# Kernel tuning notes

Hardware: AMD Instinct MI355X
Metric: run time of the kernel (lower is better)

## Reference

```python
import jax, jax.numpy as jnp
import numpy as np

N = 100000
E = 1600000
D = 64
ED = 16
L = 3


def setup_inputs() -> dict:
    key = jax.random.key(0)
    ks = jax.random.split(key, 12)
    s = 1.0 / np.sqrt(D)
    se = 1.0 / np.sqrt(ED)
    return {
        "x": jax.random.normal(ks[0], (N, D), dtype=jnp.float32),
        "edge_index": jax.random.randint(ks[1], (2, E), 0, N, dtype=jnp.int64),
        "edge_attr": jax.random.normal(ks[2], (E, ED), dtype=jnp.float32),
        "Wk": jax.random.normal(ks[3], (L, D, D), dtype=jnp.float32) * s,
        "bk": jnp.zeros((L, D), dtype=jnp.float32),
        "Wq": jax.random.normal(ks[4], (L, D, D), dtype=jnp.float32) * s,
        "bq": jnp.zeros((L, D), dtype=jnp.float32),
        "Wv": jax.random.normal(ks[5], (L, D, D), dtype=jnp.float32) * s,
        "bv": jnp.zeros((L, D), dtype=jnp.float32),
        "We": jax.random.normal(ks[6], (L, ED, D), dtype=jnp.float32) * se,
        "be": jnp.zeros((L, D), dtype=jnp.float32),
        "Wskip": jax.random.normal(ks[7], (L, D, D), dtype=jnp.float32) * s,
        "bias": jnp.zeros((L, D), dtype=jnp.float32),
        "Wl": jax.random.normal(ks[8], (D, 1), dtype=jnp.float32) * s,
        "bl": jnp.zeros((1,), dtype=jnp.float32),
    }


def _res_gated_conv(h, src, dst, edge_attr, Wk, bk, Wq, bq, Wv, bv, We, be, Wskip, bias):
    # PyG ResGatedGraphConv: eta = sigmoid(k_i + q_j + lin_edge(e)); out_i = sum_j eta * v_j + lin_skip(x_i) + bias
    k = h @ Wk + bk            # [N, D]
    q = h @ Wq + bq            # [N, D]
    v = h @ Wv + bv            # [N, D]
    e = edge_attr @ We + be    # [E, D]
    gate = jax.nn.sigmoid(k[dst] + q[src] + e)   # [E, D]
    msg = gate * v[src]                          # [E, D]
    agg = jax.ops.segment_sum(msg, dst, num_segments=N)  # scatter-add to targets
    return agg + h @ Wskip + bias


def reference(x, edge_index, edge_attr, Wk, bk, Wq, bq, Wv, bv, We, be, Wskip, bias, Wl, bl):
    src = edge_index[0]  # j (source, flow source_to_target)
    dst = edge_index[1]  # i (target)
    h = x
    h = jax.nn.elu(_res_gated_conv(h, src, dst, edge_attr, Wk[0], bk[0], Wq[0], bq[0], Wv[0], bv[0], We[0], be[0], Wskip[0], bias[0]))
    feat = jax.nn.elu(_res_gated_conv(h, src, dst, edge_attr, Wk[1], bk[1], Wq[1], bq[1], Wv[1], bv[1], We[1], be[1], Wskip[1], bias[1]))
    h = jax.nn.elu(_res_gated_conv(feat, src, dst, edge_attr, Wk[2], bk[2], Wq[2], bq[2], Wv[2], bv[2], We[2], be[2], Wskip[2], bias[2]))
    logits = h @ Wl + bl                         # [N, 1]
    return (jax.nn.sigmoid(logits), feat, jnp.concatenate((feat, logits), axis=1))
```

## Files before the change

### kernel.cpp

```cpp
#include <hip/hip_runtime.h>
#include <hip/hip_bf16.h>
#include <math.h>


#define D_CH 64
#define E_CH 16

__global__ void k_prep(const unsigned int* __restrict__ ei, int* __restrict__ flag,
                       int* __restrict__ deg, int N, int nsamp) {
  int i = blockIdx.x * blockDim.x + threadIdx.x;
  if (i < N) deg[i] = 0;
  if (blockIdx.x == 0) {
    unsigned int acc = 0;
    for (int s = threadIdx.x; s < nsamp; s += blockDim.x) acc |= ei[2 * s + 1];
    int nz = __syncthreads_or(acc != 0u);
    if (threadIdx.x == 0) flag[0] = nz ? 0 : 1;
  }
}

__global__ void k_normhist(const void* __restrict__ ei, const int* __restrict__ flag,
                           int* __restrict__ src, int* __restrict__ dstA,
                           int* __restrict__ deg, int E) {
  int e = blockIdx.x * blockDim.x + threadIdx.x;
  if (e >= E) return;
  int s, d;
  if (flag[0]) {
    const long long* p = (const long long*)ei;
    s = (int)p[e];
    d = (int)p[E + e];
  } else {
    const int* p = (const int*)ei;
    s = p[e];
    d = p[E + e];
  }
  src[e] = s;
  dstA[e] = d;
  atomicAdd(&deg[d], 1);
}

__global__ void k_scanpart(const int* __restrict__ deg, int* __restrict__ partial, int N) {
  __shared__ int wsum[4];
  int tid = threadIdx.x, lane = tid & 63, w = tid >> 6;
  int i0 = blockIdx.x * 1024 + tid * 4;
  int4 v = make_int4(0, 0, 0, 0);
  if (i0 + 3 < N) {
    v = *(const int4*)(deg + i0);
  } else {
    if (i0 < N) v.x = deg[i0];
    if (i0 + 1 < N) v.y = deg[i0 + 1];
    if (i0 + 2 < N) v.z = deg[i0 + 2];
  }
  int s = v.x + v.y + v.z + v.w;
#pragma unroll
  for (int m = 32; m; m >>= 1) s += __shfl_xor(s, m);
  if (lane == 0) wsum[w] = s;
  __syncthreads();
  if (tid == 0) partial[blockIdx.x] = wsum[0] + wsum[1] + wsum[2] + wsum[3];
}

__global__ void k_scanroot(int* __restrict__ partial, int* __restrict__ offsets,
                           int NB, int N) {
  if (NB <= 128) {
    int lane = threadIdx.x;
    int a = (lane < NB) ? partial[lane] : 0;
    int b = (lane + 64 < NB) ? partial[lane + 64] : 0;
    int sa = a, sb = b;
#pragma unroll
    for (int off = 1; off < 64; off <<= 1) {
      int t = __shfl_up(sa, off);
      if (lane >= off) sa += t;
      int u = __shfl_up(sb, off);
      if (lane >= off) sb += u;
    }
    int atot = __shfl(sa, 63);
    sb += atot;
    int tot = __shfl(sb, 63);
    if (lane < NB) partial[lane] = sa - a;
    if (lane + 64 < NB) partial[lane + 64] = sb - b;
    if (lane == 0) offsets[N] = tot;
  } else {
    if (threadIdx.x == 0) {
      int run = 0;
      for (int bI = 0; bI < NB; ++bI) {
        int vv = partial[bI];
        partial[bI] = run;
        run += vv;
      }
      offsets[N] = run;
    }
  }
}

__global__ void k_scanapply(const int* __restrict__ deg, const int* __restrict__ partial,
                            int* __restrict__ offsets, int* __restrict__ cursor, int N) {
  __shared__ int wsum[4];
  int tid = threadIdx.x, lane = tid & 63, w = tid >> 6;
  int i0 = blockIdx.x * 1024 + tid * 4;
  int4 v = make_int4(0, 0, 0, 0);
  if (i0 + 3 < N) {
    v = *(const int4*)(deg + i0);
  } else {
    if (i0 < N) v.x = deg[i0];
    if (i0 + 1 < N) v.y = deg[i0 + 1];
    if (i0 + 2 < N) v.z = deg[i0 + 2];
  }
  int ts = v.x + v.y + v.z + v.w;
  int s = ts;
#pragma unroll
  for (int off = 1; off < 64; off <<= 1) {
    int t = __shfl_up(s, off);
    if (lane >= off) s += t;
  }
  if (lane == 63) wsum[w] = s;
  __syncthreads();
  int wb = 0;
#pragma unroll
  for (int x = 0; x < 4; ++x)
    if (x < w) wb += wsum[x];
  int excl = s - ts + wb + partial[blockIdx.x];
  int o0 = excl, o1 = o0 + v.x, o2 = o1 + v.y, o3 = o2 + v.z;
  if (i0 + 3 < N) {
    int4 o = make_int4(o0, o1, o2, o3);
    *(int4*)(offsets + i0) = o;
    *(int4*)(cursor + i0) = o;
  } else {
    if (i0 < N) { offsets[i0] = o0; cursor[i0] = o0; }
    if (i0 + 1 < N) { offsets[i0 + 1] = o1; cursor[i0 + 1] = o1; }
    if (i0 + 2 < N) { offsets[i0 + 2] = o2; cursor[i0 + 2] = o2; }
  }
}

__global__ void k_scatter(const int* __restrict__ src, const int* __restrict__ dstA,
                          int* __restrict__ cursor, int2* __restrict__ je, int E) {
  int e = blockIdx.x * blockDim.x + threadIdx.x;
  if (e >= E) return;
  int d = dstA[e];
  int p = atomicAdd(&cursor[d], 1);
  je[p] = make_int2(src[e], e);
}

__device__ __forceinline__ float bcastf(float v, int srclane) {
  return __int_as_float(__builtin_amdgcn_readlane(__float_as_int(v), srclane));
}

__global__ __launch_bounds__(256, 1) void k_nodelin(
    const float* __restrict__ hin, const float* __restrict__ Wa,
    const float* __restrict__ ba, const float* __restrict__ Wb,
    const float* __restrict__ bb, float* __restrict__ outa, float* __restrict__ outb,
    int ostride, int N) {
  int lane = threadIdx.x & 63;
  int wave = blockIdx.x * (blockDim.x >> 6) + (threadIdx.x >> 6);
  int nwaves = gridDim.x * (blockDim.x >> 6);
  float wa[64], wb[64];
#pragma unroll
  for (int c = 0; c < 64; ++c) {
    wa[c] = Wa[c * 64 + lane];
    wb[c] = Wb[c * 64 + lane];
  }
  float bav = ba[lane], bbv = bb[lane];
  for (int i = wave; i < N; i += nwaves) {
    float h = hin[(size_t)i * 64 + lane];
    float a = bav, b = bbv;
#pragma unroll
    for (int c = 0; c < 64; ++c) {
      float hc = bcastf(h, c);
      a = fmaf(hc, wa[c], a);
      b = fmaf(hc, wb[c], b);
    }
    outa[(size_t)i * ostride + lane] = a;
    outb[(size_t)i * ostride + lane] = b;
  }
}

#define EDGE_LOAD(K, T)                                                        \
  int j##K = __builtin_amdgcn_readlane(meta.x, (T));                           \
  int eI##K = __builtin_amdgcn_readlane(meta.y, (T));                          \
  const float4* ap##K = (const float4*)(ea + (size_t)eI##K * E_CH);            \
  float4 eA##K##a = ap##K[0], eA##K##b = ap##K[1], eA##K##c = ap##K[2],        \
         eA##K##d = ap##K[3];                                                  \
  float q##K = qv[(size_t)j##K * 128 + lane];                                  \
  float v##K = qv[(size_t)j##K * 128 + 64 + lane];

#define EDGE_COMP(K)                                                           \
  {                                                                            \
    float ev = 0.f;                                                            \
    ev = fmaf(eA##K##a.x, we[0], ev);                                          \
    ev = fmaf(eA##K##a.y, we[1], ev);                                          \
    ev = fmaf(eA##K##a.z, we[2], ev);                                          \
    ev = fmaf(eA##K##a.w, we[3], ev);                                          \
    ev = fmaf(eA##K##b.x, we[4], ev);                                          \
    ev = fmaf(eA##K##b.y, we[5], ev);                                          \
    ev = fmaf(eA##K##b.z, we[6], ev);                                          \
    ev = fmaf(eA##K##b.w, we[7], ev);                                          \
    ev = fmaf(eA##K##c.x, we[8], ev);                                          \
    ev = fmaf(eA##K##c.y, we[9], ev);                                          \
    ev = fmaf(eA##K##c.z, we[10], ev);                                         \
    ev = fmaf(eA##K##c.w, we[11], ev);                                         \
    ev = fmaf(eA##K##d.x, we[12], ev);                                         \
    ev = fmaf(eA##K##d.y, we[13], ev);                                         \
    ev = fmaf(eA##K##d.z, we[14], ev);                                         \
    ev = fmaf(eA##K##d.w, we[15], ev);                                         \
    float g = ki + q##K + ev;                                                  \
    g = 1.0f / (1.0f + __expf(-g));                                            \
    acc = fmaf(g, v##K, acc);                                                  \
  }

template <int MODE>
__global__ __launch_bounds__(256, 3) void k_edge(
    const int* __restrict__ offsets, const int2* __restrict__ je,
    const float* __restrict__ kk, const float* __restrict__ qv,
    const float* __restrict__ base, const float* __restrict__ ea,
    const float* __restrict__ We, const float* __restrict__ be,
    float* __restrict__ hnext, float* __restrict__ dout,
    const float* __restrict__ Wl, const float* __restrict__ bl, int N) {
  int lane = threadIdx.x & 63;
  int wave = blockIdx.x * (blockDim.x >> 6) + (threadIdx.x >> 6);
  int nwaves = gridDim.x * (blockDim.x >> 6);
  float we[16];
#pragma unroll
  for (int c = 0; c < 16; ++c) we[c] = We[c * 64 + lane];
  float bev = be[lane];
  float wl = (MODE == 2) ? Wl[lane] : 0.f;
  float bl0 = (MODE == 2) ? bl[0] : 0.f;
  for (int i = wave; i < N; i += nwaves) {
    float ki = kk[(size_t)i * 64 + lane] + bev;
    float acc = base[(size_t)i * 64 + lane];
    int p0 = __builtin_amdgcn_readfirstlane(offsets[i]);
    int p1 = __builtin_amdgcn_readfirstlane(offsets[i + 1]);
    for (int pb = p0; pb < p1; pb += 64) {
      int m = p1 - pb;
      if (m > 64) m = 64;
      int idx = pb + ((lane < m) ? lane : 0);
      int2 meta = je[idx];
      int t = 0;
      for (; t + 4 <= m; t += 4) {
        EDGE_LOAD(0, t)
        EDGE_LOAD(1, t + 1)
        EDGE_LOAD(2, t + 2)
        EDGE_LOAD(3, t + 3)
        EDGE_COMP(0)
        EDGE_COMP(1)
        EDGE_COMP(2)
        EDGE_COMP(3)
      }
      for (; t < m; ++t) {
        EDGE_LOAD(5, t)
        EDGE_COMP(5)
      }
    }
    float r = (acc > 0.f) ? acc : expm1f(acc);
    if (MODE == 0) {
      hnext[(size_t)i * 64 + lane] = r;
    } else if (MODE == 1) {
      hnext[(size_t)i * 64 + lane] = r;
      dout[(size_t)N + (size_t)i * 64 + lane] = r;
      dout[(size_t)N * 65 + (size_t)i * 65 + lane] = r;
    } else {
      float dot = r * wl;
#pragma unroll
      for (int m2 = 32; m2 >= 1; m2 >>= 1) dot += __shfl_xor(dot, m2);
      float logit = dot + bl0;
      if (lane == 0) {
        dout[i] = 1.0f / (1.0f + __expf(-logit));
        dout[(size_t)N * 65 + (size_t)i * 65 + 64] = logit;
      }
    }
  }
}

extern "C" void kernel_launch(void* const* d_in, const int* in_sizes, int n_in,
                              void* d_out, int out_size, void* d_ws, size_t ws_size,
                              hipStream_t stream) {
  const float* x   = (const float*)d_in[0];
  const void*  ei  = d_in[1];
  const float* ea  = (const float*)d_in[2];
  const float* Wk  = (const float*)d_in[3];
  const float* bk  = (const float*)d_in[4];
  const float* Wq  = (const float*)d_in[5];
  const float* bq  = (const float*)d_in[6];
  const float* Wv  = (const float*)d_in[7];
  const float* bv  = (const float*)d_in[8];
  const float* We  = (const float*)d_in[9];
  const float* be  = (const float*)d_in[10];
  const float* Ws  = (const float*)d_in[11];
  const float* bia = (const float*)d_in[12];
  const float* Wl  = (const float*)d_in[13];
  const float* bl  = (const float*)d_in[14];
  int N = in_sizes[0] / D_CH;
  int E = in_sizes[2] / E_CH;
  int NB = (N + 1023) / 1024;

  char* w = (char*)d_ws;
  auto alloc = [&](size_t bytes) -> char* {
    char* r = w;
    w += (bytes + 255) & ~(size_t)255;
    return r;
  };
  int* flag     = (int*)alloc(16);
  int* src      = (int*)alloc((size_t)E * 4);
  int* dstA     = (int*)alloc((size_t)E * 4);
  int* deg      = (int*)alloc((size_t)N * 4);
  int* partial  = (int*)alloc((size_t)NB * 4);
  int* offsets  = (int*)alloc((size_t)(N + 1) * 4);
  int* cursor   = (int*)alloc((size_t)N * 4);
  int2* je      = (int2*)alloc((size_t)E * 8);
  float* kk     = (float*)alloc((size_t)N * D_CH * 4);
  float* qv     = (float*)alloc((size_t)N * 128 * 4);
  float* baseb  = (float*)alloc((size_t)N * D_CH * 4);
  float* h1     = (float*)alloc((size_t)N * D_CH * 4);
  float* feat   = (float*)alloc((size_t)N * D_CH * 4);
  float* dout   = (float*)d_out;

  int gE = (E + 255) / 256;
  int gN = (N + 255) / 256;

  k_prep<<<gN, 256, 0, stream>>>((const unsigned int*)ei, flag, deg, N, 8192);
  k_normhist<<<gE, 256, 0, stream>>>(ei, flag, src, dstA, deg, E);
  k_scanpart<<<NB, 256, 0, stream>>>(deg, partial, N);
  k_scanroot<<<1, 64, 0, stream>>>(partial, offsets, NB, N);
  k_scanapply<<<NB, 256, 0, stream>>>(deg, partial, offsets, cursor, N);
  k_scatter<<<gE, 256, 0, stream>>>(src, dstA, cursor, je, E);

  const float* hin = x;
  for (int l = 0; l < 3; ++l) {
    const float* Wk_l = Wk + (size_t)l * 4096;
    const float* bk_l = bk + (size_t)l * 64;
    const float* Wq_l = Wq + (size_t)l * 4096;
    const float* bq_l = bq + (size_t)l * 64;
    const float* Wv_l = Wv + (size_t)l * 4096;
    const float* bv_l = bv + (size_t)l * 64;
    const float* We_l = We + (size_t)l * 1024;
    const float* be_l = be + (size_t)l * 64;
    const float* Ws_l = Ws + (size_t)l * 4096;
    const float* bi_l = bia + (size_t)l * 64;

    k_nodelin<<<1024, 256, 0, stream>>>(hin, Wk_l, bk_l, Ws_l, bi_l, kk, baseb, 64, N);
    k_nodelin<<<1024, 256, 0, stream>>>(hin, Wq_l, bq_l, Wv_l, bv_l, qv, qv + 64, 128, N);
    if (l == 0) {
      k_edge<0><<<2048, 256, 0, stream>>>(offsets, je, kk, qv, baseb, ea, We_l, be_l,
                                          h1, dout, Wl, bl, N);
      hin = h1;
    } else if (l == 1) {
      k_edge<1><<<2048, 256, 0, stream>>>(offsets, je, kk, qv, baseb, ea, We_l, be_l,
                                          feat, dout, Wl, bl, N);
      hin = feat;
    } else {
      k_edge<2><<<2048, 256, 0, stream>>>(offsets, je, kk, qv, baseb, ea, We_l, be_l,
                                          h1, dout, Wl, bl, N);
    }
  }
}
```

Baseline: 1.270 ms.

## Interleave q/v per channel and batch 16 neighbor gathers per edge iteration

The q and v node projections are now stored interleaved per channel, so the edge kernel fetches both with one float2 load per neighbor instead of two separate loads. The edge loop is unrolled to 16 neighbors, and all q/v gathers are issued before a scheduling barrier so more memory requests are in flight before the gate math. The occupancy hint rises from 3 to 4 blocks per CU. The deeper batch raises register pressure, which may conflict with the higher occupancy target and cause spills. Nodes with fewer than 16 neighbors go through the scalar tail loop.

```diff
diff --git a/kernel.cpp b/kernel.cpp
--- a/kernel.cpp
+++ b/kernel.cpp
@@ -147,7 +147,7 @@
     const float* __restrict__ hin, const float* __restrict__ Wa,
     const float* __restrict__ ba, const float* __restrict__ Wb,
     const float* __restrict__ bb, float* __restrict__ outa, float* __restrict__ outb,
-    int ostride, int N) {
+    int ostride, int astep, int N) {
   int lane = threadIdx.x & 63;
   int wave = blockIdx.x * (blockDim.x >> 6) + (threadIdx.x >> 6);
   int nwaves = gridDim.x * (blockDim.x >> 6);
@@ -167,46 +167,13 @@
       a = fmaf(hc, wa[c], a);
       b = fmaf(hc, wb[c], b);
     }
-    outa[(size_t)i * ostride + lane] = a;
-    outb[(size_t)i * ostride + lane] = b;
-  }
-}
-
-#define EDGE_LOAD(K, T)                                                        \
-  int j##K = __builtin_amdgcn_readlane(meta.x, (T));                           \
-  int eI##K = __builtin_amdgcn_readlane(meta.y, (T));                          \
-  const float4* ap##K = (const float4*)(ea + (size_t)eI##K * E_CH);            \
-  float4 eA##K##a = ap##K[0], eA##K##b = ap##K[1], eA##K##c = ap##K[2],        \
-         eA##K##d = ap##K[3];                                                  \
-  float q##K = qv[(size_t)j##K * 128 + lane];                                  \
-  float v##K = qv[(size_t)j##K * 128 + 64 + lane];
-
-#define EDGE_COMP(K)                                                           \
-  {                                                                            \
-    float ev = 0.f;                                                            \
-    ev = fmaf(eA##K##a.x, we[0], ev);                                          \
-    ev = fmaf(eA##K##a.y, we[1], ev);                                          \
-    ev = fmaf(eA##K##a.z, we[2], ev);                                          \
-    ev = fmaf(eA##K##a.w, we[3], ev);                                          \
-    ev = fmaf(eA##K##b.x, we[4], ev);                                          \
-    ev = fmaf(eA##K##b.y, we[5], ev);                                          \
-    ev = fmaf(eA##K##b.z, we[6], ev);                                          \
-    ev = fmaf(eA##K##b.w, we[7], ev);                                          \
-    ev = fmaf(eA##K##c.x, we[8], ev);                                          \
-    ev = fmaf(eA##K##c.y, we[9], ev);                                          \
-    ev = fmaf(eA##K##c.z, we[10], ev);                                         \
-    ev = fmaf(eA##K##c.w, we[11], ev);                                         \
-    ev = fmaf(eA##K##d.x, we[12], ev);                                         \
-    ev = fmaf(eA##K##d.y, we[13], ev);                                         \
-    ev = fmaf(eA##K##d.z, we[14], ev);                                         \
-    ev = fmaf(eA##K##d.w, we[15], ev);                                         \
-    float g = ki + q##K + ev;                                                  \
-    g = 1.0f / (1.0f + __expf(-g));                                            \
-    acc = fmaf(g, v##K, acc);                                                  \
-  }
+    outa[(size_t)i * ostride + astep * lane] = a;
+    outb[(size_t)i * ostride + astep * lane] = b;
+  }
+}
 
 template <int MODE>
-__global__ __launch_bounds__(256, 3) void k_edge(
+__global__ __launch_bounds__(256, 4) void k_edge(
     const int* __restrict__ offsets, const int2* __restrict__ je,
     const float* __restrict__ kk, const float* __restrict__ qv,
     const float* __restrict__ base, const float* __restrict__ ea,
@@ -233,19 +200,52 @@
       int idx = pb + ((lane < m) ? lane : 0);
       int2 meta = je[idx];
       int t = 0;
-      for (; t + 4 <= m; t += 4) {
-        EDGE_LOAD(0, t)
-        EDGE_LOAD(1, t + 1)
-        EDGE_LOAD(2, t + 2)
-        EDGE_LOAD(3, t + 3)
-        EDGE_COMP(0)
-        EDGE_COMP(1)
-        EDGE_COMP(2)
-        EDGE_COMP(3)
+      for (; t + 16 <= m; t += 16) {
+        float2 qvr[16];
+        int eidv[16];
+#pragma unroll
+        for (int u = 0; u < 16; ++u) {
+          int j = __builtin_amdgcn_readlane(meta.x, t + u);
+          eidv[u] = __builtin_amdgcn_readlane(meta.y, t + u);
+          qvr[u] = *(const float2*)(qv + (size_t)j * 128 + 2 * lane);
+        }
+        __builtin_amdgcn_sched_barrier(0);
+#pragma unroll
+        for (int u = 0; u < 16; ++u) {
+          const float4* ap = (const float4*)(ea + (size_t)eidv[u] * E_CH);
+          float4 a0 = ap[0], a1 = ap[1], a2 = ap[2], a3 = ap[3];
+          float ev = 0.f;
+          ev = fmaf(a0.x, we[0], ev);   ev = fmaf(a0.y, we[1], ev);
+          ev = fmaf(a0.z, we[2], ev);   ev = fmaf(a0.w, we[3], ev);
+          ev = fmaf(a1.x, we[4], ev);   ev = fmaf(a1.y, we[5], ev);
+          ev = fmaf(a1.z, we[6], ev);   ev = fmaf(a1.w, we[7], ev);
+          ev = fmaf(a2.x, we[8], ev);   ev = fmaf(a2.y, we[9], ev);
+          ev = fmaf(a2.z, we[10], ev);  ev = fmaf(a2.w, we[11], ev);
+          ev = fmaf(a3.x, we[12], ev);  ev = fmaf(a3.y, we[13], ev);
+          ev = fmaf(a3.z, we[14], ev);  ev = fmaf(a3.w, we[15], ev);
+          float g = ki + qvr[u].x + ev;
+          g = 1.0f / (1.0f + __expf(-g));
+          acc = fmaf(g, qvr[u].y, acc);
+        }
       }
       for (; t < m; ++t) {
-        EDGE_LOAD(5, t)
-        EDGE_COMP(5)
+        int j = __builtin_amdgcn_readlane(meta.x, t);
+        int eid = __builtin_amdgcn_readlane(meta.y, t);
+        float2 qvv = *(const float2*)(qv + (size_t)j * 128 + 2 * lane);
+        const float4* ap = (const float4*)(ea + (size_t)eid * E_CH);
+        float4 a0 = ap[0], a1 = ap[1], a2 = ap[2], a3 = ap[3];
+        float ev = 0.f;
+        ev = fmaf(a0.x, we[0], ev);   ev = fmaf(a0.y, we[1], ev);
+        ev = fmaf(a0.z, we[2], ev);   ev = fmaf(a0.w, we[3], ev);
+        ev = fmaf(a1.x, we[4], ev);   ev = fmaf(a1.y, we[5], ev);
+        ev = fmaf(a1.z, we[6], ev);   ev = fmaf(a1.w, we[7], ev);
+        ev = fmaf(a2.x, we[8], ev);   ev = fmaf(a2.y, we[9], ev);
+        ev = fmaf(a2.z, we[10], ev);  ev = fmaf(a2.w, we[11], ev);
+        ev = fmaf(a3.x, we[12], ev);  ev = fmaf(a3.y, we[13], ev);
+        ev = fmaf(a3.z, we[14], ev);  ev = fmaf(a3.w, we[15], ev);
+        float g = ki + qvv.x + ev;
+        g = 1.0f / (1.0f + __expf(-g));
+        acc = fmaf(g, qvv.y, acc);
       }
     }
     float r = (acc > 0.f) ? acc : expm1f(acc);
@@ -334,8 +334,10 @@
     const float* Ws_l = Ws + (size_t)l * 4096;
     const float* bi_l = bia + (size_t)l * 64;
 
-    k_nodelin<<<1024, 256, 0, stream>>>(hin, Wk_l, bk_l, Ws_l, bi_l, kk, baseb, 64, N);
-    k_nodelin<<<1024, 256, 0, stream>>>(hin, Wq_l, bq_l, Wv_l, bv_l, qv, qv + 64, 128, N);
+    k_nodelin<<<1024, 256, 0, stream>>>(hin, Wk_l, bk_l, Ws_l, bi_l, kk, baseb,
+                                        64, 1, N);
+    k_nodelin<<<1024, 256, 0, stream>>>(hin, Wq_l, bq_l, Wv_l, bv_l, qv, qv + 1,
+                                        128, 2, N);
     if (l == 0) {
       k_edge<0><<<2048, 256, 0, stream>>>(offsets, je, kk, qv, baseb, ea, We_l, be_l,
                                           h1, dout, Wl, bl, N);
```

Result: slower. 1.426 ms (+12.3%).
